# Kernel tuning notes

Measured on AMD Instinct MI355X. Metric: run time of the kernel, lower is better.

## Reference

```python
import jax, jax.numpy as jnp
import numpy as np

EPS = 1e-5


def hetero_layernorm(x, node_type, gamma, beta):
    # LayerNorm over feature dim with per-node-type affine params.
    mu = jnp.mean(x, axis=-1, keepdims=True)
    var = jnp.mean(jnp.square(x - mu), axis=-1, keepdims=True)
    xn = (x - mu) * jax.lax.rsqrt(var + EPS)
    return xn * gamma[node_type] + beta[node_type]


def rgcn_conv(y, edge_src, edge_dst, edge_type, W_rel, W_root):
    # Transform per relation first (R small), then gather per-edge message.
    n = y.shape[0]
    h = jnp.einsum('nd,rde->rne', y, W_rel)          # [R, N, d]
    msg = h[edge_type, edge_src]                     # [E, d] gather
    agg = jax.ops.segment_sum(msg, edge_dst, num_segments=n)  # [N, d]
    return agg + y @ W_root


def hetero_mlp(y, node_type, W_mlp, b_mlp):
    # Per-node-type linear: compute for all T types, then select.
    n = y.shape[0]
    h = jnp.einsum('nd,tde->tne', y, W_mlp) + b_mlp[:, None, :]  # [T, N, d]
    return h[node_type, jnp.arange(n)]


def setup_inputs() -> dict:
    key = jax.random.key(0)
    ks = jax.random.split(key, 8)
    N, E, D, T, R = 50000, 800000, 128, 4, 8
    x = jax.random.normal(ks[0], (N, D), dtype=jnp.float32)
    edge_src = jax.random.randint(ks[1], (E,), 0, N, dtype=jnp.int32)
    edge_dst = jax.random.randint(ks[2], (E,), 0, N, dtype=jnp.int32)
    node_type = jax.random.randint(ks[3], (N,), 0, T, dtype=jnp.int32)
    edge_type = jax.random.randint(ks[4], (E,), 0, R, dtype=jnp.int32)
    # Scale weights ~ 1/sqrt(fan_in) for stable magnitudes.
    s = 1.0 / np.sqrt(D)
    W_rel = jax.random.normal(ks[5], (R, D, D), dtype=jnp.float32) * s
    W_root = jax.random.normal(ks[6], (D, D), dtype=jnp.float32) * s
    W_mlp = jax.random.normal(ks[7], (T, D, D), dtype=jnp.float32) * s
    return {
        'x': x, 'edge_src': edge_src, 'edge_dst': edge_dst,
        'node_type': node_type, 'edge_type': edge_type,
        'conv_gamma': jnp.ones((T, D), jnp.float32),
        'conv_beta': jnp.zeros((T, D), jnp.float32),
        'W_rel': W_rel, 'W_root': W_root,
        'mlp_gamma': jnp.ones((T, D), jnp.float32),
        'mlp_beta': jnp.zeros((T, D), jnp.float32),
        'W_mlp': W_mlp, 'b_mlp': jnp.zeros((T, D), jnp.float32),
    }


def reference(x, edge_src, edge_dst, node_type, edge_type,
              conv_gamma, conv_beta, W_rel, W_root,
              mlp_gamma, mlp_beta, W_mlp, b_mlp):
    # Norm -> Act -> (Dropout p=0, eval) -> Conv -> Residual
    y = hetero_layernorm(x, node_type, conv_gamma, conv_beta)
    y = jax.nn.relu(y)
    x = x + rgcn_conv(y, edge_src, edge_dst, edge_type, W_rel, W_root)
    # Norm -> Act -> (Dropout p=0, eval) -> MLP -> Residual
    y = hetero_layernorm(x, node_type, mlp_gamma, mlp_beta)
    y = jax.nn.relu(y)
    x = x + hetero_mlp(y, node_type, W_mlp, b_mlp)
    return x
```

## Files before the change

### kernel.cpp

```cpp
#include <hip/hip_runtime.h>
#include <hip/hip_bf16.h>

#define D 128
#define EPS 1e-5f
#define CHK 8192
#define P2CAP 6144

typedef __attribute__((ext_vector_type(8))) short short8;
typedef __attribute__((ext_vector_type(4))) float float4v;

__device__ inline ushort f2bf(float f) {
    __hip_bfloat16 b = __float2bfloat16(f);
    return *reinterpret_cast<ushort*>(&b);
}
__device__ inline float bf_lo(uint u) { return __uint_as_float(u << 16); }
__device__ inline float bf_hi(uint u) { return __uint_as_float(u & 0xffff0000u); }

__global__ void k_ln1(const float* __restrict__ x, const int* __restrict__ ntp,
                      const float* __restrict__ gamma, const float* __restrict__ beta,
                      ushort* __restrict__ y, int N) {
    int n = blockIdx.x * 4 + (threadIdx.x >> 6);
    if (n >= N) return;
    int l = threadIdx.x & 63;
    float2 v = *(const float2*)(x + (size_t)n * D + 2 * l);
    float s = v.x + v.y, s2 = v.x * v.x + v.y * v.y;
    #pragma unroll
    for (int o = 32; o; o >>= 1) { s += __shfl_xor(s, o, 64); s2 += __shfl_xor(s2, o, 64); }
    float mu = s * (1.0f / D);
    float var = s2 * (1.0f / D) - mu * mu;
    float inv = rsqrtf(var + EPS);
    int t = ntp[n];
    float2 g = *(const float2*)(gamma + t * D + 2 * l);
    float2 b = *(const float2*)(beta + t * D + 2 * l);
    float a0 = fmaxf((v.x - mu) * inv * g.x + b.x, 0.0f);
    float a1 = fmaxf((v.y - mu) * inv * g.y + b.y, 0.0f);
    ((uint*)(y + (size_t)n * D))[l] = ((uint)f2bf(a1) << 16) | f2bf(a0);
}

__global__ void k_cvt(const float* __restrict__ Wrel, const float* __restrict__ Wroot,
                      const float* __restrict__ Wmlp, ushort* __restrict__ Wt) {
    __shared__ ushort t[128][136];
    int m = blockIdx.x;
    const float* src = (m == 0) ? Wroot
                     : (m <= 8) ? Wrel + (size_t)(m - 1) * D * D
                                : Wmlp + (size_t)(m - 9) * D * D;
    for (int i = threadIdx.x; i < D * D; i += 256) {
        int k = i >> 7, n = i & 127;
        t[n][k] = f2bf(src[i]);
    }
    __syncthreads();
    ushort* dst = Wt + (size_t)m * D * D;
    for (int i = threadIdx.x; i < D * D; i += 256) {
        int frag = i >> 9;
        int lane = (i >> 3) & 63;
        int j = i & 7;
        int nt = frag >> 2, ks = frag & 3;
        int n = nt * 16 + (lane & 15);
        int k = ks * 32 + (lane >> 4) * 8 + j;
        dst[i] = t[n][k];
    }
}

__global__ void k_c1(const int* __restrict__ edst, int* __restrict__ hist, int E, int B) {
    __shared__ int cnt[256];
    int c = blockIdx.x, tid = threadIdx.x;
    cnt[tid] = 0;
    __syncthreads();
    #pragma unroll 4
    for (int k = 0; k < CHK / 256; ++k) {
        int e = c * CHK + k * 256 + tid;
        if (e < E) atomicAdd(&cnt[edst[e] >> 8], 1);
    }
    __syncthreads();
    if (tid < B) hist[c * B + tid] = cnt[tid];
}
__global__ void k_c2(const int* __restrict__ hist, int* __restrict__ chunkoff,
                     int* __restrict__ bucktot, int C, int B) {
    __shared__ int v[128];
    int b = blockIdx.x, t = threadIdx.x;
    v[t] = (t < C) ? hist[t * B + b] : 0;
    __syncthreads();
    if (t == 0) {
        int s = 0;
        for (int c = 0; c < C; ++c) { int x = v[c]; v[c] = s; s += x; }
        bucktot[b] = s;
    }
    __syncthreads();
    if (t < C) chunkoff[t * B + b] = v[t];
}
__global__ void k_c3(const int* __restrict__ bucktot, int* __restrict__ buckbase, int B) {
    if (threadIdx.x == 0) {
        int o = 0;
        for (int b = 0; b < B; ++b) { buckbase[b] = o; o += bucktot[b]; }
        buckbase[B] = o;
    }
}
__global__ void k_p1s(const int* __restrict__ edst, const int* __restrict__ esrc,
                      const int* __restrict__ etyp, const int* __restrict__ buckbase,
                      const int* __restrict__ chunkoff, uint* __restrict__ edata,
                      int E, int B) {
    __shared__ int base[256];
    __shared__ int cnt[256];
    int c = blockIdx.x, tid = threadIdx.x;
    if (tid < B) base[tid] = buckbase[tid] + chunkoff[c * B + tid];
    cnt[tid] = 0;
    __syncthreads();
    #pragma unroll 4
    for (int k = 0; k < CHK / 256; ++k) {
        int e = c * CHK + k * 256 + tid;
        if (e < E) {
            int d = edst[e];
            int b = d >> 8;
            int r = atomicAdd(&cnt[b], 1);
            edata[base[b] + r] =
                ((uint)esrc[e] << 12) | ((uint)(d & 255) << 4) | (uint)etyp[e];
        }
    }
}
__global__ void k_p2(const uint* __restrict__ edata, const int* __restrict__ buckbase,
                     uint* __restrict__ epack, int* __restrict__ offs,
                     int N, int E, int B) {
    __shared__ uint ed[P2CAP];
    __shared__ int cnt[256], off[256], cur[256];
    int b = blockIdx.x, tid = threadIdx.x;
    int j0 = buckbase[b];
    int count = buckbase[b + 1] - j0;
    if (count > P2CAP) count = P2CAP;
    for (int i = tid; i < count; i += 256) ed[i] = edata[j0 + i];
    cnt[tid] = 0;
    __syncthreads();
    for (int i = tid; i < count; i += 256) atomicAdd(&cnt[(ed[i] >> 4) & 255], 1);
    __syncthreads();
    if (tid == 0) {
        int s = 0;
        for (int i = 0; i < 256; ++i) { off[i] = s; cur[i] = s; s += cnt[i]; }
    }
    __syncthreads();
    for (int i = tid; i < count; i += 256) {
        uint v = ed[i];
        int dl = (v >> 4) & 255;
        int r = atomicAdd(&cur[dl], 1);
        epack[j0 + r] = ((v & 15u) << 28) | (v >> 12);
    }
    int v = b * 256 + tid;
    if (v < N) offs[v] = j0 + off[tid];
    if (b == 0 && tid == 0) offs[N] = E;
}

__global__ void k_zagg(const ushort* __restrict__ ybuf, const int* __restrict__ offs,
                       const uint* __restrict__ epack, ushort* __restrict__ zbuf, int N) {
    int wave = threadIdx.x >> 6;
    int l = threadIdx.x & 63;
    int v = blockIdx.x * 4 + wave;
    if (v >= N) return;
    float2 a0 = {0.f,0.f}, a1 = {0.f,0.f}, a2 = {0.f,0.f}, a3 = {0.f,0.f};
    float2 a4 = {0.f,0.f}, a5 = {0.f,0.f}, a6 = {0.f,0.f}, a7 = {0.f,0.f};
    const uint* yb = (const uint*)ybuf;
    int j = offs[v], e1 = offs[v + 1];

#define ZACC(P, U) do {                                                   \
        float lo = bf_lo(U), hi = bf_hi(U);                               \
        switch ((P) >> 28) {                                              \
            case 0: a0.x += lo; a0.y += hi; break;                        \
            case 1: a1.x += lo; a1.y += hi; break;                        \
            case 2: a2.x += lo; a2.y += hi; break;                        \
            case 3: a3.x += lo; a3.y += hi; break;                        \
            case 4: a4.x += lo; a4.y += hi; break;                        \
            case 5: a5.x += lo; a5.y += hi; break;                        \
            case 6: a6.x += lo; a6.y += hi; break;                        \
            default: a7.x += lo; a7.y += hi; break;                       \
        }                                                                 \
    } while (0)

    while (j < e1) {
        int chunk = min(64, e1 - j);
        uint pl = (j + l < e1) ? epack[j + l] : 0;
        int i = 0;
        for (; i + 3 < chunk; i += 4) {
            uint p0 = __shfl(pl, i, 64);
            uint p1 = __shfl(pl, i + 1, 64);
            uint p2 = __shfl(pl, i + 2, 64);
            uint p3 = __shfl(pl, i + 3, 64);
            uint u0 = yb[(size_t)(p0 & 0x0FFFFFFFu) * 64 + l];
            uint u1 = yb[(size_t)(p1 & 0x0FFFFFFFu) * 64 + l];
            uint u2 = yb[(size_t)(p2 & 0x0FFFFFFFu) * 64 + l];
            uint u3 = yb[(size_t)(p3 & 0x0FFFFFFFu) * 64 + l];
            ZACC(p0, u0); ZACC(p1, u1); ZACC(p2, u2); ZACC(p3, u3);
        }
        for (; i < chunk; ++i) {
            uint p = __shfl(pl, i, 64);
            uint u = yb[(size_t)(p & 0x0FFFFFFFu) * 64 + l];
            ZACC(p, u);
        }
        j += chunk;
    }
#undef ZACC
    uint* zrow = (uint*)(zbuf + (size_t)v * 1024);
    zrow[0 * 64 + l] = ((uint)f2bf(a0.y) << 16) | f2bf(a0.x);
    zrow[1 * 64 + l] = ((uint)f2bf(a1.y) << 16) | f2bf(a1.x);
    zrow[2 * 64 + l] = ((uint)f2bf(a2.y) << 16) | f2bf(a2.x);
    zrow[3 * 64 + l] = ((uint)f2bf(a3.y) << 16) | f2bf(a3.x);
    zrow[4 * 64 + l] = ((uint)f2bf(a4.y) << 16) | f2bf(a4.x);
    zrow[5 * 64 + l] = ((uint)f2bf(a5.y) << 16) | f2bf(a5.x);
    zrow[6 * 64 + l] = ((uint)f2bf(a6.y) << 16) | f2bf(a6.x);
    zrow[7 * 64 + l] = ((uint)f2bf(a7.y) << 16) | f2bf(a7.x);
}

__launch_bounds__(256)
__global__ void k_gemm2(const ushort* __restrict__ ybuf, const ushort* __restrict__ zbuf,
                        const ushort* __restrict__ Wt, const float* __restrict__ x,
                        const int* __restrict__ ntp,
                        const float* __restrict__ gamma, const float* __restrict__ beta,
                        float* __restrict__ x2, ushort* __restrict__ y2, int N) {
    __shared__ ushort wsm[16384];
    int tid = threadIdx.x;
    int wave = tid >> 6, lane = tid & 63;
    int quad = lane >> 4, l15 = lane & 15;
    int base = blockIdx.x * 64 + wave * 16;
    int arow = min(base + l15, N - 1);
    const ushort* yrow = ybuf + (size_t)arow * 128;
    const ushort* zrow = zbuf + (size_t)arow * 1024;

    float4v acc[8];
    #pragma unroll
    for (int nt = 0; nt < 8; ++nt) acc[nt] = (float4v){0.f, 0.f, 0.f, 0.f};

    for (int mat = 0; mat < 9; ++mat) {
        __syncthreads();
        const ushort* wsrc = Wt + (size_t)mat * 16384;
        #pragma unroll
        for (int jj = 0; jj < 8; ++jj)
            *(uint4*)(wsm + jj * 2048 + tid * 8) = *(const uint4*)(wsrc + jj * 2048 + tid * 8);
        __syncthreads();
        const ushort* ap = (mat == 0) ? yrow : zrow + (mat - 1) * 128;
        short8 a[4];
        #pragma unroll
        for (int ks = 0; ks < 4; ++ks) a[ks] = *(const short8*)(ap + ks * 32 + quad * 8);
        #pragma unroll
        for (int nt = 0; nt < 8; ++nt) {
            #pragma unroll
            for (int ks = 0; ks < 4; ++ks) {
                short8 b = *(const short8*)(wsm + (((nt * 4 + ks) * 64 + lane) << 3));
                acc[nt] = __builtin_amdgcn_mfma_f32_16x16x32_bf16(a[ks], b, acc[nt], 0, 0, 0);
            }
        }
    }

    float s[4] = {0.f, 0.f, 0.f, 0.f}, s2[4] = {0.f, 0.f, 0.f, 0.f};
    #pragma unroll
    for (int nt = 0; nt < 8; ++nt) {
        int col = nt * 16 + l15;
        #pragma unroll
        for (int r = 0; r < 4; ++r) {
            int row = base + quad * 4 + r;
            float xv = (row < N) ? x[(size_t)row * D + col] : 0.f;
            float t = acc[nt][r] + xv;
            acc[nt][r] = t;
            s[r] += t; s2[r] += t * t;
        }
    }
    #pragma unroll
    for (int r = 0; r < 4; ++r) {
        #pragma unroll
        for (int o = 1; o < 16; o <<= 1) {
            s[r]  += __shfl_xor(s[r],  o, 64);
            s2[r] += __shfl_xor(s2[r], o, 64);
        }
    }
    #pragma unroll
    for (int r = 0; r < 4; ++r) {
        int row = base + quad * 4 + r;
        int rc = min(row, N - 1);
        int t = ntp[rc];
        float mu  = s[r] * (1.0f / D);
        float var = s2[r] * (1.0f / D) - mu * mu;
        float inv = rsqrtf(var + EPS);
        #pragma unroll
        for (int nt = 0; nt < 8; ++nt) {
            int col = nt * 16 + l15;
            float xx = acc[nt][r];
            float yn = fmaxf((xx - mu) * inv * gamma[t * D + col] + beta[t * D + col], 0.f);
            if (row < N) {
                x2[(size_t)row * D + col] = xx;
                y2[(size_t)row * D + col] = f2bf(yn);
            }
        }
    }
}

__global__ void k_mlp(const ushort* __restrict__ y2, const float* __restrict__ x2,
                      const int* __restrict__ ntp,
                      const ushort* __restrict__ Wt, const float* __restrict__ bmlp,
                      float* __restrict__ out, int N) {
    int wave = threadIdx.x >> 6;
    int lane = threadIdx.x & 63;
    int quad = lane >> 4, l15 = lane & 15;
    int base = blockIdx.x * 64 + wave * 16;
    int arow = min(base + l15, N - 1);
    short8 a[4];
    const ushort* yrow = y2 + (size_t)arow * D + quad * 8;
    #pragma unroll
    for (int ks = 0; ks < 4; ++ks) a[ks] = *(const short8*)(yrow + ks * 32);
    int ty[4];
    #pragma unroll
    for (int r = 0; r < 4; ++r) ty[r] = ntp[min(base + quad * 4 + r, N - 1)];
    const ushort* W0 = Wt + (size_t)9  * D * D;
    const ushort* W1 = Wt + (size_t)10 * D * D;
    const ushort* W2 = Wt + (size_t)11 * D * D;
    const ushort* W3 = Wt + (size_t)12 * D * D;
    #pragma unroll
    for (int nt = 0; nt < 8; ++nt) {
        float4v c0 = {0.f,0.f,0.f,0.f}, c1 = {0.f,0.f,0.f,0.f};
        float4v c2 = {0.f,0.f,0.f,0.f}, c3 = {0.f,0.f,0.f,0.f};
        #pragma unroll
        for (int ks = 0; ks < 4; ++ks) {
            int fo = ((nt * 4 + ks) * 64 + lane) << 3;
            short8 b0 = *(const short8*)(W0 + fo);
            short8 b1 = *(const short8*)(W1 + fo);
            short8 b2 = *(const short8*)(W2 + fo);
            short8 b3 = *(const short8*)(W3 + fo);
            c0 = __builtin_amdgcn_mfma_f32_16x16x32_bf16(a[ks], b0, c0, 0, 0, 0);
            c1 = __builtin_amdgcn_mfma_f32_16x16x32_bf16(a[ks], b1, c1, 0, 0, 0);
            c2 = __builtin_amdgcn_mfma_f32_16x16x32_bf16(a[ks], b2, c2, 0, 0, 0);
            c3 = __builtin_amdgcn_mfma_f32_16x16x32_bf16(a[ks], b3, c3, 0, 0, 0);
        }
        int col = nt * 16 + l15;
        #pragma unroll
        for (int r = 0; r < 4; ++r) {
            int row = base + quad * 4 + r;
            if (row < N) {
                int t = ty[r];
                float v = (t == 0) ? c0[r] : (t == 1) ? c1[r] : (t == 2) ? c2[r] : c3[r];
                out[(size_t)row * D + col] =
                    x2[(size_t)row * D + col] + v + bmlp[t * D + col];
            }
        }
    }
}

extern "C" void kernel_launch(void* const* d_in, const int* in_sizes, int n_in,
                              void* d_out, int out_size, void* d_ws, size_t ws_size,
                              hipStream_t stream) {
    const float* x          = (const float*)d_in[0];
    const int*   esrc       = (const int*)d_in[1];
    const int*   edst       = (const int*)d_in[2];
    const int*   ntyp       = (const int*)d_in[3];
    const int*   etyp       = (const int*)d_in[4];
    const float* conv_gamma = (const float*)d_in[5];
    const float* conv_beta  = (const float*)d_in[6];
    const float* W_rel      = (const float*)d_in[7];
    const float* W_root     = (const float*)d_in[8];
    const float* mlp_gamma  = (const float*)d_in[9];
    const float* mlp_beta   = (const float*)d_in[10];
    const float* W_mlp      = (const float*)d_in[11];
    const float* b_mlp      = (const float*)d_in[12];
    float* out = (float*)d_out;

    int N = in_sizes[0] / D;
    int E = in_sizes[1];
    int C = (E + CHK - 1) / CHK;
    int B = (N + 255) / 256;

    char* p = (char*)d_ws;
    auto take = [&p](size_t bytes) { char* q = p; p += (bytes + 255) & ~(size_t)255; return q; };
    ushort* ybuf    = (ushort*)take((size_t)N * D * 2);
    ushort* y2      = (ushort*)take((size_t)N * D * 2);
    ushort* zbuf    = (ushort*)take((size_t)N * 1024 * 2);
    float*  x2      = (float*)take((size_t)N * D * 4);
    ushort* Wt      = (ushort*)take((size_t)13 * D * D * 2);
    uint*   edata   = (uint*)take((size_t)E * 4);
    uint*   epack   = (uint*)take((size_t)E * 4);
    int*    offs    = (int*)take((size_t)(N + 1) * 4);
    int*    hist    = (int*)take((size_t)C * B * 4);
    int*    chunkoff= (int*)take((size_t)C * B * 4);
    int*    bucktot = (int*)take((size_t)B * 4);
    int*    buckbase= (int*)take((size_t)(B + 1) * 4);

    k_ln1<<<(N + 3) / 4, 256, 0, stream>>>(x, ntyp, conv_gamma, conv_beta, ybuf, N);
    k_cvt<<<13, 256, 0, stream>>>(W_rel, W_root, W_mlp, Wt);

    k_c1<<<C, 256, 0, stream>>>(edst, hist, E, B);
    k_c2<<<B, 128, 0, stream>>>(hist, chunkoff, bucktot, C, B);
    k_c3<<<1, 64, 0, stream>>>(bucktot, buckbase, B);
    k_p1s<<<C, 256, 0, stream>>>(edst, esrc, etyp, buckbase, chunkoff, edata, E, B);
    k_p2<<<B, 256, 0, stream>>>(edata, buckbase, epack, offs, N, E, B);

    k_zagg<<<(N + 3) / 4, 256, 0, stream>>>(ybuf, offs, epack, zbuf, N);

    k_gemm2<<<(N + 63) / 64, 256, 0, stream>>>(ybuf, zbuf, Wt, x, ntyp,
                                               mlp_gamma, mlp_beta, x2, y2, N);

    k_mlp<<<(N + 63) / 64, 256, 0, stream>>>(y2, x2, ntyp, Wt, b_mlp, out, N);
}
```

Before: 292.1 us.

## Fuse conv GEMM with MLP, merge LN1 with weight convert, inline bucket scan

Merges the conv GEMM and hetero-MLP kernels so the second LayerNorm output stays in shared memory and the residual stays in registers. This removes the fp32 x2 and bf16 y2 round trips through global memory. The weight conversion is folded into the LN1 launch as 13 extra blocks. The single-thread bucket-base scan kernel is replaced by a block-level prefix scan repeated inside the partition kernels. Together these cut three launches and roughly 38 MB of intermediate traffic, at the cost of redundant per-block scans and a larger fused kernel whose register pressure may lower occupancy.

```diff
diff --git a/kernel.cpp b/kernel.cpp
--- a/kernel.cpp
+++ b/kernel.cpp
@@ -16,10 +16,35 @@
 __device__ inline float bf_lo(uint u) { return __uint_as_float(u << 16); }
 __device__ inline float bf_hi(uint u) { return __uint_as_float(u & 0xffff0000u); }
 
-__global__ void k_ln1(const float* __restrict__ x, const int* __restrict__ ntp,
-                      const float* __restrict__ gamma, const float* __restrict__ beta,
-                      ushort* __restrict__ y, int N) {
-    int n = blockIdx.x * 4 + (threadIdx.x >> 6);
+__global__ void k_ln1cvt(const float* __restrict__ x, const int* __restrict__ ntp,
+                         const float* __restrict__ gamma, const float* __restrict__ beta,
+                         ushort* __restrict__ y,
+                         const float* __restrict__ Wrel, const float* __restrict__ Wroot,
+                         const float* __restrict__ Wmlp, ushort* __restrict__ Wt, int N) {
+    __shared__ ushort t[128][136];
+    if (blockIdx.x < 13) {
+        int m = blockIdx.x;
+        const float* src = (m == 0) ? Wroot
+                         : (m <= 8) ? Wrel + (size_t)(m - 1) * D * D
+                                    : Wmlp + (size_t)(m - 9) * D * D;
+        for (int i = threadIdx.x; i < D * D; i += 256) {
+            int k = i >> 7, n = i & 127;
+            t[n][k] = f2bf(src[i]);
+        }
+        __syncthreads();
+        ushort* dst = Wt + (size_t)m * D * D;
+        for (int i = threadIdx.x; i < D * D; i += 256) {
+            int frag = i >> 9;
+            int lane = (i >> 3) & 63;
+            int j = i & 7;
+            int nt = frag >> 2, ks = frag & 3;
+            int n = nt * 16 + (lane & 15);
+            int k = ks * 32 + (lane >> 4) * 8 + j;
+            dst[i] = t[n][k];
+        }
+        return;
+    }
+    int n = (blockIdx.x - 13) * 4 + (threadIdx.x >> 6);
     if (n >= N) return;
     int l = threadIdx.x & 63;
     float2 v = *(const float2*)(x + (size_t)n * D + 2 * l);
@@ -29,36 +54,12 @@
     float mu = s * (1.0f / D);
     float var = s2 * (1.0f / D) - mu * mu;
     float inv = rsqrtf(var + EPS);
-    int t = ntp[n];
-    float2 g = *(const float2*)(gamma + t * D + 2 * l);
-    float2 b = *(const float2*)(beta + t * D + 2 * l);
+    int tt = ntp[n];
+    float2 g = *(const float2*)(gamma + tt * D + 2 * l);
+    float2 b = *(const float2*)(beta + tt * D + 2 * l);
     float a0 = fmaxf((v.x - mu) * inv * g.x + b.x, 0.0f);
     float a1 = fmaxf((v.y - mu) * inv * g.y + b.y, 0.0f);
     ((uint*)(y + (size_t)n * D))[l] = ((uint)f2bf(a1) << 16) | f2bf(a0);
-}
-
-__global__ void k_cvt(const float* __restrict__ Wrel, const float* __restrict__ Wroot,
-                      const float* __restrict__ Wmlp, ushort* __restrict__ Wt) {
-    __shared__ ushort t[128][136];
-    int m = blockIdx.x;
-    const float* src = (m == 0) ? Wroot
-                     : (m <= 8) ? Wrel + (size_t)(m - 1) * D * D
-                                : Wmlp + (size_t)(m - 9) * D * D;
-    for (int i = threadIdx.x; i < D * D; i += 256) {
-        int k = i >> 7, n = i & 127;
-        t[n][k] = f2bf(src[i]);
-    }
-    __syncthreads();
-    ushort* dst = Wt + (size_t)m * D * D;
-    for (int i = threadIdx.x; i < D * D; i += 256) {
-        int frag = i >> 9;
-        int lane = (i >> 3) & 63;
-        int j = i & 7;
-        int nt = frag >> 2, ks = frag & 3;
-        int n = nt * 16 + (lane & 15);
-        int k = ks * 32 + (lane >> 4) * 8 + j;
-        dst[i] = t[n][k];
-    }
 }
 
 __global__ void k_c1(const int* __restrict__ edst, int* __restrict__ hist, int E, int B) {
@@ -88,21 +89,24 @@
     __syncthreads();
     if (t < C) chunkoff[t * B + b] = v[t];
 }
-__global__ void k_c3(const int* __restrict__ bucktot, int* __restrict__ buckbase, int B) {
-    if (threadIdx.x == 0) {
-        int o = 0;
-        for (int b = 0; b < B; ++b) { buckbase[b] = o; o += bucktot[b]; }
-        buckbase[B] = o;
-    }
-}
 __global__ void k_p1s(const int* __restrict__ edst, const int* __restrict__ esrc,
-                      const int* __restrict__ etyp, const int* __restrict__ buckbase,
+                      const int* __restrict__ etyp, const int* __restrict__ bucktot,
                       const int* __restrict__ chunkoff, uint* __restrict__ edata,
                       int E, int B) {
+    __shared__ int ps[256];
     __shared__ int base[256];
     __shared__ int cnt[256];
     int c = blockIdx.x, tid = threadIdx.x;
-    if (tid < B) base[tid] = buckbase[tid] + chunkoff[c * B + tid];
+    int bt = (tid < B) ? bucktot[tid] : 0;
+    ps[tid] = bt;
+    __syncthreads();
+    for (int o = 1; o < 256; o <<= 1) {
+        int v = (tid >= o) ? ps[tid - o] : 0;
+        __syncthreads();
+        ps[tid] += v;
+        __syncthreads();
+    }
+    base[tid] = (ps[tid] - bt) + ((tid < B) ? chunkoff[c * B + tid] : 0);
     cnt[tid] = 0;
     __syncthreads();
     #pragma unroll 4
@@ -117,14 +121,24 @@
         }
     }
 }
-__global__ void k_p2(const uint* __restrict__ edata, const int* __restrict__ buckbase,
+__global__ void k_p2(const uint* __restrict__ edata, const int* __restrict__ bucktot,
                      uint* __restrict__ epack, int* __restrict__ offs,
                      int N, int E, int B) {
+    __shared__ int ps[256];
     __shared__ uint ed[P2CAP];
     __shared__ int cnt[256], off[256], cur[256];
     int b = blockIdx.x, tid = threadIdx.x;
-    int j0 = buckbase[b];
-    int count = buckbase[b + 1] - j0;
+    int bt = (tid < B) ? bucktot[tid] : 0;
+    ps[tid] = bt;
+    __syncthreads();
+    for (int o = 1; o < 256; o <<= 1) {
+        int v = (tid >= o) ? ps[tid - o] : 0;
+        __syncthreads();
+        ps[tid] += v;
+        __syncthreads();
+    }
+    int j0 = ps[b] - ((b < B) ? bucktot[b] : 0);
+    int count = ps[b] - j0;
     if (count > P2CAP) count = P2CAP;
     for (int i = tid; i < count; i += 256) ed[i] = edata[j0 + i];
     cnt[tid] = 0;
@@ -207,11 +221,11 @@
 }
 
 __launch_bounds__(256)
-__global__ void k_gemm2(const ushort* __restrict__ ybuf, const ushort* __restrict__ zbuf,
-                        const ushort* __restrict__ Wt, const float* __restrict__ x,
-                        const int* __restrict__ ntp,
-                        const float* __restrict__ gamma, const float* __restrict__ beta,
-                        float* __restrict__ x2, ushort* __restrict__ y2, int N) {
+__global__ void k_gm(const ushort* __restrict__ ybuf, const ushort* __restrict__ zbuf,
+                     const ushort* __restrict__ Wt, const float* __restrict__ x,
+                     const int* __restrict__ ntp,
+                     const float* __restrict__ gamma, const float* __restrict__ beta,
+                     const float* __restrict__ bmlp, float* __restrict__ out, int N) {
     __shared__ ushort wsm[16384];
     int tid = threadIdx.x;
     int wave = tid >> 6, lane = tid & 63;
@@ -246,6 +260,7 @@
         }
     }
 
+    __syncthreads();
     float s[4] = {0.f, 0.f, 0.f, 0.f}, s2[4] = {0.f, 0.f, 0.f, 0.f};
     #pragma unroll
     for (int nt = 0; nt < 8; ++nt) {
@@ -267,43 +282,28 @@
             s2[r] += __shfl_xor(s2[r], o, 64);
         }
     }
+    int ty[4];
     #pragma unroll
     for (int r = 0; r < 4; ++r) {
-        int row = base + quad * 4 + r;
-        int rc = min(row, N - 1);
-        int t = ntp[rc];
+        int rc = min(base + quad * 4 + r, N - 1);
+        ty[r] = ntp[rc];
         float mu  = s[r] * (1.0f / D);
         float var = s2[r] * (1.0f / D) - mu * mu;
         float inv = rsqrtf(var + EPS);
+        int lrow = wave * 16 + quad * 4 + r;
         #pragma unroll
         for (int nt = 0; nt < 8; ++nt) {
             int col = nt * 16 + l15;
-            float xx = acc[nt][r];
-            float yn = fmaxf((xx - mu) * inv * gamma[t * D + col] + beta[t * D + col], 0.f);
-            if (row < N) {
-                x2[(size_t)row * D + col] = xx;
-                y2[(size_t)row * D + col] = f2bf(yn);
-            }
-        }
-    }
-}
-
-__global__ void k_mlp(const ushort* __restrict__ y2, const float* __restrict__ x2,
-                      const int* __restrict__ ntp,
-                      const ushort* __restrict__ Wt, const float* __restrict__ bmlp,
-                      float* __restrict__ out, int N) {
-    int wave = threadIdx.x >> 6;
-    int lane = threadIdx.x & 63;
-    int quad = lane >> 4, l15 = lane & 15;
-    int base = blockIdx.x * 64 + wave * 16;
-    int arow = min(base + l15, N - 1);
-    short8 a[4];
-    const ushort* yrow = y2 + (size_t)arow * D + quad * 8;
-    #pragma unroll
-    for (int ks = 0; ks < 4; ++ks) a[ks] = *(const short8*)(yrow + ks * 32);
-    int ty[4];
-    #pragma unroll
-    for (int r = 0; r < 4; ++r) ty[r] = ntp[min(base + quad * 4 + r, N - 1)];
+            float yn = fmaxf((acc[nt][r] - mu) * inv * gamma[ty[r] * D + col]
+                             + beta[ty[r] * D + col], 0.f);
+            wsm[lrow * 136 + col] = f2bf(yn);
+        }
+    }
+    short8 a2[4];
+    const ushort* myrow = wsm + (wave * 16 + l15) * 136;
+    #pragma unroll
+    for (int ks = 0; ks < 4; ++ks) a2[ks] = *(const short8*)(myrow + ks * 32 + quad * 8);
+
     const ushort* W0 = Wt + (size_t)9  * D * D;
     const ushort* W1 = Wt + (size_t)10 * D * D;
     const ushort* W2 = Wt + (size_t)11 * D * D;
@@ -319,10 +319,10 @@
             short8 b1 = *(const short8*)(W1 + fo);
             short8 b2 = *(const short8*)(W2 + fo);
             short8 b3 = *(const short8*)(W3 + fo);
-            c0 = __builtin_amdgcn_mfma_f32_16x16x32_bf16(a[ks], b0, c0, 0, 0, 0);
-            c1 = __builtin_amdgcn_mfma_f32_16x16x32_bf16(a[ks], b1, c1, 0, 0, 0);
-            c2 = __builtin_amdgcn_mfma_f32_16x16x32_bf16(a[ks], b2, c2, 0, 0, 0);
-            c3 = __builtin_amdgcn_mfma_f32_16x16x32_bf16(a[ks], b3, c3, 0, 0, 0);
+            c0 = __builtin_amdgcn_mfma_f32_16x16x32_bf16(a2[ks], b0, c0, 0, 0, 0);
+            c1 = __builtin_amdgcn_mfma_f32_16x16x32_bf16(a2[ks], b1, c1, 0, 0, 0);
+            c2 = __builtin_amdgcn_mfma_f32_16x16x32_bf16(a2[ks], b2, c2, 0, 0, 0);
+            c3 = __builtin_amdgcn_mfma_f32_16x16x32_bf16(a2[ks], b3, c3, 0, 0, 0);
         }
         int col = nt * 16 + l15;
         #pragma unroll
@@ -331,8 +331,7 @@
             if (row < N) {
                 int t = ty[r];
                 float v = (t == 0) ? c0[r] : (t == 1) ? c1[r] : (t == 2) ? c2[r] : c3[r];
-                out[(size_t)row * D + col] =
-                    x2[(size_t)row * D + col] + v + bmlp[t * D + col];
+                out[(size_t)row * D + col] = acc[nt][r] + v + bmlp[t * D + col];
             }
         }
     }
@@ -364,9 +363,7 @@
     char* p = (char*)d_ws;
     auto take = [&p](size_t bytes) { char* q = p; p += (bytes + 255) & ~(size_t)255; return q; };
     ushort* ybuf    = (ushort*)take((size_t)N * D * 2);
-    ushort* y2      = (ushort*)take((size_t)N * D * 2);
     ushort* zbuf    = (ushort*)take((size_t)N * 1024 * 2);
-    float*  x2      = (float*)take((size_t)N * D * 4);
     ushort* Wt      = (ushort*)take((size_t)13 * D * D * 2);
     uint*   edata   = (uint*)take((size_t)E * 4);
     uint*   epack   = (uint*)take((size_t)E * 4);
@@ -374,21 +371,17 @@
     int*    hist    = (int*)take((size_t)C * B * 4);
     int*    chunkoff= (int*)take((size_t)C * B * 4);
     int*    bucktot = (int*)take((size_t)B * 4);
-    int*    buckbase= (int*)take((size_t)(B + 1) * 4);
-
-    k_ln1<<<(N + 3) / 4, 256, 0, stream>>>(x, ntyp, conv_gamma, conv_beta, ybuf, N);
-    k_cvt<<<13, 256, 0, stream>>>(W_rel, W_root, W_mlp, Wt);
+
+    k_ln1cvt<<<13 + (N + 3) / 4, 256, 0, stream>>>(x, ntyp, conv_gamma, conv_beta,
+                                                   ybuf, W_rel, W_root, W_mlp, Wt, N);
 
     k_c1<<<C, 256, 0, stream>>>(edst, hist, E, B);
     k_c2<<<B, 128, 0, stream>>>(hist, chunkoff, bucktot, C, B);
-    k_c3<<<1, 64, 0, stream>>>(bucktot, buckbase, B);
-    k_p1s<<<C, 256, 0, stream>>>(edst, esrc, etyp, buckbase, chunkoff, edata, E, B);
-    k_p2<<<B, 256, 0, stream>>>(edata, buckbase, epack, offs, N, E, B);
+    k_p1s<<<C, 256, 0, stream>>>(edst, esrc, etyp, bucktot, chunkoff, edata, E, B);
+    k_p2<<<B, 256, 0, stream>>>(edata, bucktot, epack, offs, N, E, B);
 
     k_zagg<<<(N + 3) / 4, 256, 0, stream>>>(ybuf, offs, epack, zbuf, N);
 
-    k_gemm2<<<(N + 63) / 64, 256, 0, stream>>>(ybuf, zbuf, Wt, x, ntyp,
-                                               mlp_gamma, mlp_beta, x2, y2, N);
-
-    k_mlp<<<(N + 63) / 64, 256, 0, stream>>>(y2, x2, ntyp, Wt, b_mlp, out, N);
-}
+    k_gm<<<(N + 63) / 64, 256, 0, stream>>>(ybuf, zbuf, Wt, x, ntyp,
+                                            mlp_gamma, mlp_beta, b_mlp, out, N);
+}
```

Measured after the change: 289.5 us. About the same (-0.9%).
